# Kernel tuning notes

Measured on AMD Instinct MI355X. Metric: run time of the kernel, lower is better.

## Reference

```python
import jax, jax.numpy as jnp
import numpy as np
from jax import lax

INPUT_SCALE = 1.0
RES_SCALE = 1.0


def setup_inputs() -> dict:
    key = jax.random.key(0)
    k1, k2, k3, k4 = jax.random.split(key, 4)
    seq_len, input_size, res_size = 4096, 512, 2048
    return {
        "input_data": jax.random.normal(k1, (seq_len, input_size), dtype=jnp.float32),
        "initial_state": jax.random.normal(k2, (res_size,), dtype=jnp.float32),
        "W_in": jax.random.normal(k3, (res_size, input_size), dtype=jnp.float32),
        "W_res": jax.random.normal(k4, (res_size, res_size), dtype=jnp.float32),
    }


def reference(input_data, initial_state, W_in, W_res):
    # state_t = tanh(input_scale * W_in @ x_t + res_scale * W_res @ state_{t-1}) / sqrt(res_size)
    res_size = W_res.shape[0]
    inv_sqrt = jnp.asarray(1.0 / np.sqrt(res_size), dtype=input_data.dtype)
    # Precompute input projection for all timesteps as one GEMM: (seq_len, res_size)
    pre = (INPUT_SCALE * input_data) @ W_in.T

    def step(state, u_t):
        new_state = jnp.tanh(u_t + RES_SCALE * (W_res @ state)) * inv_sqrt
        return new_state, new_state

    _, states = lax.scan(step, initial_state, pre)
    # (seq_len + 1, res_size): row 0 is the initial state
    return jnp.concatenate([initial_state[None, :], states], axis=0)
```

## Files before the change

kernel.cpp:

```cpp
#include <hip/hip_runtime.h>

constexpr int SEQ   = 4096;
constexpr int IN    = 512;
constexpr int RS    = 2048;
constexpr int GB    = 64;
constexpr int BT    = 512;
constexpr int RING  = 8;
constexpr int NCOPY = 8;
constexpr int CSTR32 = RING * RS;
constexpr int CSTR64 = RING * RS / 2;
constexpr float INV_SQRT = 0.022097086912079612f;

__device__ __forceinline__ float fast_tanh(float x) {
    float e = __expf(2.0f * x);
    return 1.0f - 2.0f * __builtin_amdgcn_rcpf(e + 1.0f);
}

typedef unsigned long long u64;
#define AT_LOAD_U64(p)     __hip_atomic_load((p), __ATOMIC_RELAXED, __HIP_MEMORY_SCOPE_AGENT)
#define AT_STORE_U32(p, v) __hip_atomic_store((p), (v), __ATOMIC_RELAXED, __HIP_MEMORY_SCOPE_AGENT)

__global__ __launch_bounds__(BT, 2)
void reservoir_scan_kernel(const float* __restrict__ x,
                           const float* __restrict__ init,
                           const float* __restrict__ W_in,
                           const float* __restrict__ W_res,
                           float* __restrict__ out,
                           unsigned* __restrict__ ring32) {
    __shared__ float s_state[RS];
    __shared__ float s_pub[32];
    u64* ring = (u64*)ring32;
    const int bid  = blockIdx.x;
    const int tid  = threadIdx.x;
    const int wave = tid >> 6;
    const int lane = tid & 63;
    const int r0   = bid * 32 + wave * 4;
    const int myc  = bid & (NCOPY - 1);

    float4 w[4][8];
#pragma unroll
    for (int r = 0; r < 4; ++r) {
        const float* wp = W_res + (size_t)(r0 + r) * RS + lane * 4;
#pragma unroll
        for (int j = 0; j < 8; ++j) w[r][j] = *(const float4*)(wp + j * 256);
    }
#pragma unroll
    for (int r = 0; r < 4; ++r)
#pragma unroll
        for (int j = 0; j < 8; ++j)
            asm volatile("" : "+v"(w[r][j].x), "+v"(w[r][j].y),
                              "+v"(w[r][j].z), "+v"(w[r][j].w));

    float4 wi[4][2];
#pragma unroll
    for (int r = 0; r < 4; ++r) {
        const float* wp = W_in + (size_t)(r0 + r) * IN + lane * 8;
        wi[r][0] = *(const float4*)wp;
        wi[r][1] = *(const float4*)(wp + 4);
    }
#pragma unroll
    for (int r = 0; r < 4; ++r)
#pragma unroll
        for (int j = 0; j < 2; ++j)
            asm volatile("" : "+v"(wi[r][j].x), "+v"(wi[r][j].y),
                              "+v"(wi[r][j].z), "+v"(wi[r][j].w));

    if (wave == 0 && lane < 32) {
        float v = init[bid * 32 + lane];
        out[bid * 32 + lane] = v;
        s_pub[lane] = v;
#pragma unroll
        for (int c = 0; c < NCOPY; ++c)
            AT_STORE_U32(ring32 + c * CSTR32 + bid * 32 + lane,
                         __float_as_uint(v) | 1u);
    }
    __syncthreads();

    for (int t = 0; t < SEQ; ++t) {
        const size_t crow = (size_t)(t & (RING - 1)) * (RS / 2);
        const size_t prow = (size_t)((t + 1) & (RING - 1)) * RS;
        const unsigned tag_c = ((unsigned)(t >> 3) & 1u) ^ 1u;
        const unsigned tag_p = ((unsigned)((t + 1) >> 3) & 1u) ^ 1u;

        const float* xp = x + (size_t)t * IN + lane * 8;
        float4 xv0 = *(const float4*)xp;
        float4 xv1 = *(const float4*)(xp + 4);

        if ((tid >> 3) == bid) {
            const int k = tid & 7;
            *(float4*)&s_state[4 * tid] = *(const float4*)&s_pub[4 * k];
        } else {
            const u64* pp = ring + myc * CSTR64 + crow + 2 * tid;
            u64 v0 = AT_LOAD_U64(pp);
            u64 v1 = AT_LOAD_U64(pp + 1);
#define RDY(v) (((((unsigned)(v) ^ tag_c) | ((unsigned)((v) >> 32) ^ tag_c)) & 1u) == 0u)
            while (!(RDY(v0) && RDY(v1))) {
                v0 = AT_LOAD_U64(pp);
                v1 = AT_LOAD_U64(pp + 1);
            }
#undef RDY
            float4 sv;
            sv.x = __uint_as_float((unsigned)v0);
            sv.y = __uint_as_float((unsigned)(v0 >> 32));
            sv.z = __uint_as_float((unsigned)v1);
            sv.w = __uint_as_float((unsigned)(v1 >> 32));
            *(float4*)&s_state[4 * tid] = sv;
        }
        __syncthreads();

        float a0 = wi[0][0].x*xv0.x + wi[0][0].y*xv0.y + wi[0][0].z*xv0.z + wi[0][0].w*xv0.w
                 + wi[0][1].x*xv1.x + wi[0][1].y*xv1.y + wi[0][1].z*xv1.z + wi[0][1].w*xv1.w;
        float a1 = wi[1][0].x*xv0.x + wi[1][0].y*xv0.y + wi[1][0].z*xv0.z + wi[1][0].w*xv0.w
                 + wi[1][1].x*xv1.x + wi[1][1].y*xv1.y + wi[1][1].z*xv1.z + wi[1][1].w*xv1.w;
        float a2 = wi[2][0].x*xv0.x + wi[2][0].y*xv0.y + wi[2][0].z*xv0.z + wi[2][0].w*xv0.w
                 + wi[2][1].x*xv1.x + wi[2][1].y*xv1.y + wi[2][1].z*xv1.z + wi[2][1].w*xv1.w;
        float a3 = wi[3][0].x*xv0.x + wi[3][0].y*xv0.y + wi[3][0].z*xv0.z + wi[3][0].w*xv0.w
                 + wi[3][1].x*xv1.x + wi[3][1].y*xv1.y + wi[3][1].z*xv1.z + wi[3][1].w*xv1.w;
#pragma unroll
        for (int j = 0; j < 8; ++j) {
            const float4 sv = *(const float4*)&s_state[lane * 4 + j * 256];
            a0 += w[0][j].x * sv.x + w[0][j].y * sv.y + w[0][j].z * sv.z + w[0][j].w * sv.w;
            a1 += w[1][j].x * sv.x + w[1][j].y * sv.y + w[1][j].z * sv.z + w[1][j].w * sv.w;
            a2 += w[2][j].x * sv.x + w[2][j].y * sv.y + w[2][j].z * sv.z + w[2][j].w * sv.w;
            a3 += w[3][j].x * sv.x + w[3][j].y * sv.y + w[3][j].z * sv.z + w[3][j].w * sv.w;
        }

        const bool p1 = (lane & 1) != 0;
        float k01 = p1 ? a1 : a0, s01 = p1 ? a0 : a1;
        k01 += __shfl_xor(s01, 1);
        float k23 = p1 ? a3 : a2, s23 = p1 ? a2 : a3;
        k23 += __shfl_xor(s23, 1);
        const bool p2 = (lane & 2) != 0;
        float kk = p2 ? k23 : k01, ss = p2 ? k01 : k23;
        kk += __shfl_xor(ss, 2);
        kk += __shfl_xor(kk, 4);
        kk += __shfl_xor(kk, 8);
        kk += __shfl_xor(kk, 16);
        kk += __shfl_xor(kk, 32);

        float sres = 0.f;
        if (lane < 4) {
            sres = fast_tanh(kk) * INV_SQRT;
            s_pub[wave * 4 + lane] = sres;
        }
        __syncthreads();

        if (wave == 0 && lane < 32) {
            unsigned bits = (__float_as_uint(s_pub[lane]) & ~1u) | tag_p;
#pragma unroll
            for (int c = 0; c < NCOPY; ++c)
                AT_STORE_U32(ring32 + c * CSTR32 + prow + bid * 32 + lane, bits);
        }

        if (lane < 4)
            out[(size_t)(t + 1) * RS + r0 + lane] = sres;
    }
}

extern "C" void kernel_launch(void* const* d_in, const int* in_sizes, int n_in,
                              void* d_out, int out_size, void* d_ws, size_t ws_size,
                              hipStream_t stream) {
    const float* x     = (const float*)d_in[0];
    const float* init  = (const float*)d_in[1];
    const float* W_in  = (const float*)d_in[2];
    const float* W_res = (const float*)d_in[3];
    float* out = (float*)d_out;
    unsigned* ring = (unsigned*)d_ws;

    hipMemsetAsync(d_ws, 0, (size_t)NCOPY * RING * RS * sizeof(float), stream);

    void* args[] = { (void*)&x, (void*)&init, (void*)&W_in, (void*)&W_res,
                     (void*)&out, (void*)&ring };
    hipLaunchCooperativeKernel((void*)reservoir_scan_kernel,
                               dim3(GB), dim3(BT), args, 0, stream);
}
```

Baseline: 7.925 ms.

## Replace end-of-step block barrier with last-wave-publishes counter, single ring copy

```diff
diff --git a/kernel.cpp b/kernel.cpp
--- a/kernel.cpp
+++ b/kernel.cpp
@@ -5,10 +5,8 @@
 constexpr int RS    = 2048;
 constexpr int GB    = 64;
 constexpr int BT    = 512;
+constexpr int WAVES = BT / 64;
 constexpr int RING  = 8;
-constexpr int NCOPY = 8;
-constexpr int CSTR32 = RING * RS;
-constexpr int CSTR64 = RING * RS / 2;
 constexpr float INV_SQRT = 0.022097086912079612f;
 
 __device__ __forceinline__ float fast_tanh(float x) {
@@ -29,13 +27,13 @@
                            unsigned* __restrict__ ring32) {
     __shared__ float s_state[RS];
     __shared__ float s_pub[32];
+    __shared__ unsigned s_cnt[2];
     u64* ring = (u64*)ring32;
     const int bid  = blockIdx.x;
     const int tid  = threadIdx.x;
     const int wave = tid >> 6;
     const int lane = tid & 63;
     const int r0   = bid * 32 + wave * 4;
-    const int myc  = bid & (NCOPY - 1);
 
     float4 w[4][8];
 #pragma unroll
@@ -65,14 +63,11 @@
             asm volatile("" : "+v"(wi[r][j].x), "+v"(wi[r][j].y),
                               "+v"(wi[r][j].z), "+v"(wi[r][j].w));
 
+    if (tid < 2) s_cnt[tid] = 0u;
     if (wave == 0 && lane < 32) {
         float v = init[bid * 32 + lane];
         out[bid * 32 + lane] = v;
-        s_pub[lane] = v;
-#pragma unroll
-        for (int c = 0; c < NCOPY; ++c)
-            AT_STORE_U32(ring32 + c * CSTR32 + bid * 32 + lane,
-                         __float_as_uint(v) | 1u);
+        AT_STORE_U32(ring32 + bid * 32 + lane, __float_as_uint(v) | 1u);
     }
     __syncthreads();
 
@@ -86,11 +81,8 @@
         float4 xv0 = *(const float4*)xp;
         float4 xv1 = *(const float4*)(xp + 4);
 
-        if ((tid >> 3) == bid) {
-            const int k = tid & 7;
-            *(float4*)&s_state[4 * tid] = *(const float4*)&s_pub[4 * k];
-        } else {
-            const u64* pp = ring + myc * CSTR64 + crow + 2 * tid;
+        {
+            const u64* pp = ring + crow + 2 * tid;
             u64 v0 = AT_LOAD_U64(pp);
             u64 v1 = AT_LOAD_U64(pp + 1);
 #define RDY(v) (((((unsigned)(v) ^ tag_c) | ((unsigned)((v) >> 32) ^ tag_c)) & 1u) == 0u)
@@ -143,13 +135,19 @@
             sres = fast_tanh(kk) * INV_SQRT;
             s_pub[wave * 4 + lane] = sres;
         }
-        __syncthreads();
 
-        if (wave == 0 && lane < 32) {
-            unsigned bits = (__float_as_uint(s_pub[lane]) & ~1u) | tag_p;
-#pragma unroll
-            for (int c = 0; c < NCOPY; ++c)
-                AT_STORE_U32(ring32 + c * CSTR32 + prow + bid * 32 + lane, bits);
+        unsigned old = 0;
+        if (lane == 0) {
+            __threadfence_block();
+            old = atomicAdd(&s_cnt[t & 1], 1u);
+        }
+        old = __shfl(old, 0);
+        if (old == (unsigned)(WAVES - 1)) {
+            if (lane == 0) s_cnt[t & 1] = 0;
+            if (lane < 32) {
+                unsigned bits = (__float_as_uint(s_pub[lane]) & ~1u) | tag_p;
+                AT_STORE_U32(ring32 + prow + bid * 32 + lane, bits);
+            }
         }
 
         if (lane < 4)
@@ -167,7 +165,7 @@
     float* out = (float*)d_out;
     unsigned* ring = (unsigned*)d_ws;
 
-    hipMemsetAsync(d_ws, 0, (size_t)NCOPY * RING * RS * sizeof(float), stream);
+    hipMemsetAsync(d_ws, 0, (size_t)RING * RS * sizeof(float), stream);
 
     void* args[] = { (void*)&x, (void*)&init, (void*)&W_in, (void*)&W_res,
                      (void*)&out, (void*)&ring };
```

Result: slower. 8.129 ms (+2.6%).
